# Kernel optimization log

Hardware: AMD Instinct MI355X
Metric: run time of the kernel (lower is better)

The kernel has to match this reference:

```python
import jax, jax.numpy as jnp
import numpy as np
from jax import lax

B, T, H, OUT = 2048, 512, 128, 64  # batch, lookback, hidden, horizon


def _p(k, shape):
    return jax.random.normal(k, shape, jnp.float32) * 0.1


def setup_inputs() -> dict:
    key = jax.random.key(0)
    ks = jax.random.split(key, 19)
    d = {"x": jax.random.normal(ks[0], (B, T), jnp.float32)}
    i = 1
    for pre in ("enc", "dec"):
        for l in range(2):
            insz = 1 if l == 0 else H
            d[f"{pre}_Wih{l}"] = _p(ks[i], (4 * H, insz)); i += 1
            d[f"{pre}_Whh{l}"] = _p(ks[i], (4 * H, H)); i += 1
            d[f"{pre}_bih{l}"] = _p(ks[i], (4 * H,)); i += 1
            d[f"{pre}_bhh{l}"] = _p(ks[i], (4 * H,)); i += 1
    d["lin_W"] = _p(ks[17], (1, H))
    d["lin_b"] = _p(ks[18], (1,))
    return d


def _cell(x, h, c, Wih, Whh, bih, bhh):
    # PyTorch LSTM gate order: i, f, g, o
    gates = x @ Wih.T + h @ Whh.T + bih + bhh  # [B, 4H]
    i, f, g, o = jnp.split(gates, 4, axis=-1)
    c = jax.nn.sigmoid(f) * c + jax.nn.sigmoid(i) * jnp.tanh(g)
    h = jax.nn.sigmoid(o) * jnp.tanh(c)
    return h, c


def _layer(xs, Wih, Whh, bih, bhh):
    # xs: [T, B, in] -> (ys [T, B, H], final (h, c))
    b = xs.shape[1]
    h0 = jnp.zeros((b, Whh.shape[1]), xs.dtype)
    def step(carry, x):
        h, c = _cell(x, carry[0], carry[1], Wih, Whh, bih, bhh)
        return (h, c), h
    (h, c), ys = lax.scan(step, (h0, h0), xs)
    return ys, (h, c)


def reference(x,
              enc_Wih0, enc_Whh0, enc_bih0, enc_bhh0,
              enc_Wih1, enc_Whh1, enc_bih1, enc_bhh1,
              dec_Wih0, dec_Whh0, dec_bih0, dec_bhh0,
              dec_Wih1, dec_Whh1, dec_bih1, dec_bhh1,
              lin_W, lin_b):
    xs = x.T[:, :, None]  # [T, B, 1]
    ys0, (h0, c0) = _layer(xs, enc_Wih0, enc_Whh0, enc_bih0, enc_bhh0)
    _,   (h1, c1) = _layer(ys0, enc_Wih1, enc_Whh1, enc_bih1, enc_bhh1)

    inp0 = x[:, -1:]  # [B, 1] last observed price
    def dec_step(carry, _):
        inp, a, b_, h, c = carry
        a, b_ = _cell(inp, a, b_, dec_Wih0, dec_Whh0, dec_bih0, dec_bhh0)
        h, c = _cell(a, h, c, dec_Wih1, dec_Whh1, dec_bih1, dec_bhh1)
        pred = h @ lin_W.T + lin_b  # [B, 1]
        return (pred, a, b_, h, c), pred[:, 0]

    _, preds = lax.scan(dec_step, (inp0, h0, c0, h1, c1), None, length=OUT)
    return preds.T  # [B, OUT]
```

## Files before the change

kernel.cpp:

```cpp
#include <hip/hip_runtime.h>


typedef _Float16 half_t;
typedef _Float16 f16x8 __attribute__((ext_vector_type(8)));
typedef float    f32x4 __attribute__((ext_vector_type(4)));

#define BT   8
#define H    128
#define T    512
#define OUTS 64

__device__ __forceinline__ float sigm(float x)   { return 1.0f / (1.0f + __expf(-x)); }
__device__ __forceinline__ float tanh_f(float x) { return 2.0f / (1.0f + __expf(-2.0f * x)) - 1.0f; }

__device__ __forceinline__ void mfma_a(f32x4& d, f16x8 a, const f16x8& b) {
  asm("v_mfma_f32_16x16x32_f16 %0, %1, %2, %0" : "+v"(d) : "v"(a), "a"(b));
}
__device__ __forceinline__ void mfma_v(f32x4& d, f16x8 a, const f16x8& b) {
  asm("v_mfma_f32_16x16x32_f16 %0, %1, %2, %0" : "+v"(d) : "v"(a), "v"(b));
}

__device__ __forceinline__ f16x8 lda(const half_t* buf, int col, int kg, int kb) {
  int b  = col >> 1;
  int bc = (kb * 64 + kg * 16) ^ (b << 4);
  return *(const f16x8*)((const char*)buf + b * 256 + bc);
}

__device__ __forceinline__ void wr_h(half_t* hb, int b, int j, float h) {
  int bc = (j * 2) ^ (b << 4);
  *(half_t*)((char*)hb + b * 256 + bc) = (half_t)h;
}

template <int M>
__device__ __forceinline__ void pass_a(f32x4 (&acc)[2][4], const f16x8 (&wa)[2][4][2][4],
                                       const half_t* buf, int col, int kg) {
#pragma unroll
  for (int kb = 0; kb < 4; kb++) {
    f16x8 a = lda(buf, col, kg, kb);
#pragma unroll
    for (int jt = 0; jt < 2; jt++)
#pragma unroll
      for (int q = 0; q < 4; q++)
        mfma_a(acc[jt][q], a, wa[M][q][jt][kb]);
  }
}

__device__ __forceinline__ void pass_v(f32x4 (&acc)[2][4], const f16x8 (&wv2)[4][2][4],
                                       const half_t* buf, int col, int kg) {
#pragma unroll
  for (int kb = 0; kb < 4; kb++) {
    f16x8 a = lda(buf, col, kg, kb);
#pragma unroll
    for (int jt = 0; jt < 2; jt++)
#pragma unroll
      for (int q = 0; q < 4; q++)
        mfma_v(acc[jt][q], a, wv2[q][jt][kb]);
  }
}

__device__ __forceinline__ void zacc(f32x4 (&acc)[2][4]) {
#pragma unroll
  for (int jt = 0; jt < 2; jt++)
#pragma unroll
    for (int q = 0; q < 4; q++) acc[jt][q] = (f32x4){0.f, 0.f, 0.f, 0.f};
}

__device__ __forceinline__ void load_wa(f16x8 (&wa)[2][4][2][4], const half_t* w16,
                                        int base, int wv, int col, int kg) {
#pragma unroll
  for (int m = 0; m < 2; m++)
#pragma unroll
    for (int q = 0; q < 4; q++)
#pragma unroll
      for (int jt = 0; jt < 2; jt++)
#pragma unroll
        for (int kb = 0; kb < 4; kb++) {
          wa[m][q][jt][kb] = *(const f16x8*)(w16 + (size_t)(base + m) * 65536 +
                                             (size_t)(q * 128 + wv * 32 + jt * 16 + col) * 128 +
                                             kb * 32 + kg * 8);
          asm("" : "+a"(wa[m][q][jt][kb]));
        }
}

__device__ __forceinline__ void load_wv(f16x8 (&wv2)[4][2][4], const half_t* w16,
                                        int base, int wv, int col, int kg) {
#pragma unroll
  for (int q = 0; q < 4; q++)
#pragma unroll
    for (int jt = 0; jt < 2; jt++)
#pragma unroll
      for (int kb = 0; kb < 4; kb++)
        wv2[q][jt][kb] = *(const f16x8*)(w16 + (size_t)(base + 2) * 65536 +
                                         (size_t)(q * 128 + wv * 32 + jt * 16 + col) * 128 +
                                         kb * 32 + kg * 8);
}

__global__ void prep_kernel(const float* m0, const float* m1, const float* m2,
                            const float* m3, const float* m4, const float* m5,
                            const float* ba0, const float* bb0, const float* ba1, const float* bb1,
                            const float* ba2, const float* bb2, const float* ba3, const float* bb3,
                            const float* encWih0, const float* decWih0,
                            half_t* w16, float* biasT, float* xwT) {
  int i = blockIdx.x * 256 + threadIdx.x;
  if (i < 6 * 65536) {
    int m = i >> 16, e = i & 65535;
    const float* src = (m == 0) ? m0 : (m == 1) ? m1 : (m == 2) ? m2
                     : (m == 3) ? m3 : (m == 4) ? m4 : m5;
    w16[i] = (half_t)src[e];
  }
  if (i < 2048) {
    int set = i >> 9, wi = i & 511, q = wi >> 7, jh = wi & 127;
    const float* A  = (set == 0) ? ba0 : (set == 1) ? ba1 : (set == 2) ? ba2 : ba3;
    const float* Bv = (set == 0) ? bb0 : (set == 1) ? bb1 : (set == 2) ? bb2 : bb3;
    biasT[set * 512 + jh * 4 + q] = A[wi] + Bv[wi];
  }
  if (i < 1024) {
    int ph = i >> 9, wi = i & 511, q = wi >> 7, jh = wi & 127;
    xwT[ph * 512 + jh * 4 + q] = (ph ? decWih0 : encWih0)[wi];
  }
}

__global__ __launch_bounds__(256, 1)
void lstm_all(const float* __restrict__ x,
              const float* __restrict__ linW,
              const float* __restrict__ linb,
              const half_t* __restrict__ w16,
              const float* __restrict__ biasTg,
              const float* __restrict__ xwTg,
              float* __restrict__ out)
{
  __shared__ alignas(16) half_t h0b[2][BT * H];
  __shared__ alignas(16) half_t h1b[2][BT * H];
  __shared__ float xch[BT * 64];
  __shared__ float h1f[BT * H];
  __shared__ float linWs[H];
  __shared__ float pp[256];
  __shared__ float predbuf[BT];

  const int tid  = threadIdx.x;
  const int wv   = tid >> 6;
  const int lane = tid & 63;
  const int col  = lane & 15;
  const int kg   = lane >> 4;
  const int b0   = blockIdx.x * BT;

  for (int z = tid; z < 1024; z += 256) {
    ((unsigned*)h0b)[z] = 0u; ((unsigned*)h1b)[z] = 0u;
  }
  if (tid < H) linWs[tid] = linW[tid];

  f16x8 wa[2][4][2][4];
  f16x8 wv2[4][2][4];
  load_wa(wa, w16, 0, wv, col, kg);
  load_wv(wv2, w16, 0, wv, col, kg);

  float b0r[2][4], b1r[2][4], xwr[2][4];
#pragma unroll
  for (int jt = 0; jt < 2; jt++) {
    const int jj = wv * 32 + jt * 16 + col;
#pragma unroll
    for (int q = 0; q < 4; q++) {
      b0r[jt][q] = biasTg[jj * 4 + q];
      b1r[jt][q] = biasTg[512 + jj * 4 + q];
      xwr[jt][q] = xwTg[jj * 4 + q];
    }
  }

  float c0[2][2] = {{0, 0}, {0, 0}};
  float c1[2][2] = {{0, 0}, {0, 0}};
  int p = 0;
  __syncthreads();

  for (int tc = 0; tc < 8; tc++) {
    for (int e = tid; e < BT * 64; e += 256)
      xch[e] = x[(size_t)(b0 + (e >> 6)) * T + tc * 64 + (e & 63)];
    __syncthreads();
    for (int ti = 0; ti < 64; ti++) {
      const int np = p ^ 1;
      f32x4 acc[2][4];
      zacc(acc);
      pass_a<0>(acc, wa, h0b[p], col, kg);
#pragma unroll
      for (int jt = 0; jt < 2; jt++) {
        const int jj = wv * 32 + jt * 16 + col;
#pragma unroll
        for (int s = 0; s < 2; s++) {
          const int b = 2 * kg + s;
          const int e = 2 * s;
          float xv = xch[b * 64 + ti];
          float gi = acc[jt][0][e] + b0r[jt][0] + xv * xwr[jt][0];
          float gf = acc[jt][1][e] + b0r[jt][1] + xv * xwr[jt][1];
          float gg = acc[jt][2][e] + b0r[jt][2] + xv * xwr[jt][2];
          float go = acc[jt][3][e] + b0r[jt][3] + xv * xwr[jt][3];
          float cn = sigm(gf) * c0[jt][s] + sigm(gi) * tanh_f(gg);
          c0[jt][s] = cn;
          wr_h(h0b[np], b, jj, sigm(go) * tanh_f(cn));
        }
      }
      __syncthreads();
      zacc(acc);
      pass_v(acc, wv2, h1b[p], col, kg);
      pass_a<1>(acc, wa, h0b[np], col, kg);
#pragma unroll
      for (int jt = 0; jt < 2; jt++) {
        const int jj = wv * 32 + jt * 16 + col;
#pragma unroll
        for (int s = 0; s < 2; s++) {
          const int b = 2 * kg + s;
          const int e = 2 * s;
          float gi = acc[jt][0][e] + b1r[jt][0];
          float gf = acc[jt][1][e] + b1r[jt][1];
          float gg = acc[jt][2][e] + b1r[jt][2];
          float go = acc[jt][3][e] + b1r[jt][3];
          float cn = sigm(gf) * c1[jt][s] + sigm(gi) * tanh_f(gg);
          c1[jt][s] = cn;
          wr_h(h1b[np], b, jj, sigm(go) * tanh_f(cn));
        }
      }
      __syncthreads();
      p = np;
    }
  }

  load_wa(wa, w16, 3, wv, col, kg);
  load_wv(wv2, w16, 3, wv, col, kg);
#pragma unroll
  for (int jt = 0; jt < 2; jt++) {
    const int jj = wv * 32 + jt * 16 + col;
#pragma unroll
    for (int q = 0; q < 4; q++) {
      b0r[jt][q] = biasTg[1024 + jj * 4 + q];
      b1r[jt][q] = biasTg[1536 + jj * 4 + q];
      xwr[jt][q] = xwTg[512 + jj * 4 + q];
    }
  }
  const float lb = linb[0];
  if (tid < BT) predbuf[tid] = x[(size_t)(b0 + tid) * T + (T - 1)];
  __syncthreads();

  for (int so = 0; so < OUTS; so++) {
    const int np = p ^ 1;
    f32x4 acc[2][4];
    zacc(acc);
    pass_a<0>(acc, wa, h0b[p], col, kg);
#pragma unroll
    for (int jt = 0; jt < 2; jt++) {
      const int jj = wv * 32 + jt * 16 + col;
#pragma unroll
      for (int s = 0; s < 2; s++) {
        const int b = 2 * kg + s;
        const int e = 2 * s;
        float xv = predbuf[b];
        float gi = acc[jt][0][e] + b0r[jt][0] + xv * xwr[jt][0];
        float gf = acc[jt][1][e] + b0r[jt][1] + xv * xwr[jt][1];
        float gg = acc[jt][2][e] + b0r[jt][2] + xv * xwr[jt][2];
        float go = acc[jt][3][e] + b0r[jt][3] + xv * xwr[jt][3];
        float cn = sigm(gf) * c0[jt][s] + sigm(gi) * tanh_f(gg);
        c0[jt][s] = cn;
        wr_h(h0b[np], b, jj, sigm(go) * tanh_f(cn));
      }
    }
    __syncthreads();
    zacc(acc);
    pass_v(acc, wv2, h1b[p], col, kg);
    pass_a<1>(acc, wa, h0b[np], col, kg);
#pragma unroll
    for (int jt = 0; jt < 2; jt++) {
      const int jj = wv * 32 + jt * 16 + col;
#pragma unroll
      for (int s = 0; s < 2; s++) {
        const int b = 2 * kg + s;
        const int e = 2 * s;
        float cn = sigm(acc[jt][1][e] + b1r[jt][1]) * c1[jt][s]
                 + sigm(acc[jt][0][e] + b1r[jt][0]) * tanh_f(acc[jt][2][e] + b1r[jt][2]);
        c1[jt][s] = cn;
        float hn = sigm(acc[jt][3][e] + b1r[jt][3]) * tanh_f(cn);
        wr_h(h1b[np], b, jj, hn);
        h1f[b * H + jj] = hn;
      }
    }
    __syncthreads();
    {
      int r = tid >> 5, seg = tid & 31;
      float pv = 0.0f;
#pragma unroll
      for (int kk = 0; kk < 4; kk++) pv += h1f[r * H + seg * 4 + kk] * linWs[seg * 4 + kk];
      pp[tid] = pv;
    }
    __syncthreads();
    if (tid < BT) {
      float pv = lb;
#pragma unroll
      for (int g2 = 0; g2 < 32; g2++) pv += pp[tid * 32 + g2];
      predbuf[tid] = pv;
      out[(size_t)(b0 + tid) * OUTS + so] = pv;
    }
    __syncthreads();
    p = np;
  }
}

extern "C" void kernel_launch(void* const* d_in, const int* in_sizes, int n_in,
                              void* d_out, int out_size, void* d_ws, size_t ws_size,
                              hipStream_t stream) {
  const float* x        = (const float*)d_in[0];
  const float* encWih0  = (const float*)d_in[1];
  const float* encWhh0  = (const float*)d_in[2];
  const float* encbih0  = (const float*)d_in[3];
  const float* encbhh0  = (const float*)d_in[4];
  const float* encWih1  = (const float*)d_in[5];
  const float* encWhh1  = (const float*)d_in[6];
  const float* encbih1  = (const float*)d_in[7];
  const float* encbhh1  = (const float*)d_in[8];
  const float* decWih0  = (const float*)d_in[9];
  const float* decWhh0  = (const float*)d_in[10];
  const float* decbih0  = (const float*)d_in[11];
  const float* decbhh0  = (const float*)d_in[12];
  const float* decWih1  = (const float*)d_in[13];
  const float* decWhh1  = (const float*)d_in[14];
  const float* decbih1  = (const float*)d_in[15];
  const float* decbhh1  = (const float*)d_in[16];
  const float* linW     = (const float*)d_in[17];
  const float* linb     = (const float*)d_in[18];

  half_t* w16  = (half_t*)d_ws;
  float*  biasT = (float*)((char*)d_ws + (size_t)6 * 65536 * 2);
  float*  xwT   = biasT + 2048;

  prep_kernel<<<1536, 256, 0, stream>>>(encWhh0, encWih1, encWhh1, decWhh0, decWih1, decWhh1,
                                        encbih0, encbhh0, encbih1, encbhh1,
                                        decbih0, decbhh0, decbih1, decbhh1,
                                        encWih0, decWih0, w16, biasT, xwT);
  lstm_all<<<256, 256, 0, stream>>>(x, linW, linb, w16, biasT, xwT, (float*)d_out);
}
```

Before: 1.496 ms.

## Skew encoder layers so layer1 step t runs with layer0 step t+1

Restructures the encoder recurrence as a wavefront: in each iteration, layer 1 computes step S from h0[S] while layer 0 computes step S+1 from the same buffer. The two passes then share one barrier per step instead of two, with a prologue for layer 0's first step and an epilogue for layer 1's last step. The x chunk is stored transposed so the eight batch values for a time step sit next to each other. Ping-pong buffer indices for the two layers now drift apart, so the decoder tracks separate parities p0 and p1.

```diff
diff --git a/kernel.cpp b/kernel.cpp
--- a/kernel.cpp
+++ b/kernel.cpp
@@ -131,7 +131,7 @@
 {
   __shared__ alignas(16) half_t h0b[2][BT * H];
   __shared__ alignas(16) half_t h1b[2][BT * H];
-  __shared__ float xch[BT * 64];
+  __shared__ float xch[64 * BT];
   __shared__ float h1f[BT * H];
   __shared__ float linWs[H];
   __shared__ float pp[256];
@@ -168,59 +168,117 @@
 
   float c0[2][2] = {{0, 0}, {0, 0}};
   float c1[2][2] = {{0, 0}, {0, 0}};
-  int p = 0;
+
+  for (int e = tid; e < BT * 64; e += 256) {
+    int b = e >> 6, j = e & 63;
+    xch[j * 8 + b] = x[(size_t)(b0 + b) * T + j];
+  }
   __syncthreads();
 
-  for (int tc = 0; tc < 8; tc++) {
-    for (int e = tid; e < BT * 64; e += 256)
-      xch[e] = x[(size_t)(b0 + (e >> 6)) * T + tc * 64 + (e & 63)];
-    __syncthreads();
-    for (int ti = 0; ti < 64; ti++) {
-      const int np = p ^ 1;
-      f32x4 acc[2][4];
-      zacc(acc);
-      pass_a<0>(acc, wa, h0b[p], col, kg);
-#pragma unroll
-      for (int jt = 0; jt < 2; jt++) {
-        const int jj = wv * 32 + jt * 16 + col;
-#pragma unroll
-        for (int s = 0; s < 2; s++) {
-          const int b = 2 * kg + s;
-          const int e = 2 * s;
-          float xv = xch[b * 64 + ti];
-          float gi = acc[jt][0][e] + b0r[jt][0] + xv * xwr[jt][0];
-          float gf = acc[jt][1][e] + b0r[jt][1] + xv * xwr[jt][1];
-          float gg = acc[jt][2][e] + b0r[jt][2] + xv * xwr[jt][2];
-          float go = acc[jt][3][e] + b0r[jt][3] + xv * xwr[jt][3];
-          float cn = sigm(gf) * c0[jt][s] + sigm(gi) * tanh_f(gg);
-          c0[jt][s] = cn;
-          wr_h(h0b[np], b, jj, sigm(go) * tanh_f(cn));
-        }
+  {
+    f32x4 acc[2][4];
+    zacc(acc);
+    pass_a<0>(acc, wa, h0b[0], col, kg);
+#pragma unroll
+    for (int jt = 0; jt < 2; jt++) {
+      const int jj = wv * 32 + jt * 16 + col;
+#pragma unroll
+      for (int s = 0; s < 2; s++) {
+        const int b = 2 * kg + s;
+        const int e = 2 * s;
+        float xv = xch[0 * 8 + b];
+        float gi = acc[jt][0][e] + b0r[jt][0] + xv * xwr[jt][0];
+        float gf = acc[jt][1][e] + b0r[jt][1] + xv * xwr[jt][1];
+        float gg = acc[jt][2][e] + b0r[jt][2] + xv * xwr[jt][2];
+        float go = acc[jt][3][e] + b0r[jt][3] + xv * xwr[jt][3];
+        float cn = sigm(gf) * c0[jt][s] + sigm(gi) * tanh_f(gg);
+        c0[jt][s] = cn;
+        wr_h(h0b[1], b, jj, sigm(go) * tanh_f(cn));
+      }
+    }
+  }
+  __syncthreads();
+  int p = 1;
+
+  for (int S = 0; S < 511; S++) {
+    if (((S + 1) & 63) == 0) {
+      const int ch = (S + 1) >> 6;
+      for (int e = tid; e < BT * 64; e += 256) {
+        int b = e >> 6, j = e & 63;
+        xch[j * 8 + b] = x[(size_t)(b0 + b) * T + ch * 64 + j];
       }
       __syncthreads();
-      zacc(acc);
-      pass_v(acc, wv2, h1b[p], col, kg);
-      pass_a<1>(acc, wa, h0b[np], col, kg);
-#pragma unroll
-      for (int jt = 0; jt < 2; jt++) {
-        const int jj = wv * 32 + jt * 16 + col;
-#pragma unroll
-        for (int s = 0; s < 2; s++) {
-          const int b = 2 * kg + s;
-          const int e = 2 * s;
-          float gi = acc[jt][0][e] + b1r[jt][0];
-          float gf = acc[jt][1][e] + b1r[jt][1];
-          float gg = acc[jt][2][e] + b1r[jt][2];
-          float go = acc[jt][3][e] + b1r[jt][3];
-          float cn = sigm(gf) * c1[jt][s] + sigm(gi) * tanh_f(gg);
-          c1[jt][s] = cn;
-          wr_h(h1b[np], b, jj, sigm(go) * tanh_f(cn));
-        }
-      }
-      __syncthreads();
-      p = np;
-    }
-  }
+    }
+    const int np = p ^ 1;
+    f32x4 acc[2][4];
+    zacc(acc);
+    pass_v(acc, wv2, h1b[p], col, kg);
+    pass_a<1>(acc, wa, h0b[p], col, kg);
+#pragma unroll
+    for (int jt = 0; jt < 2; jt++) {
+      const int jj = wv * 32 + jt * 16 + col;
+#pragma unroll
+      for (int s = 0; s < 2; s++) {
+        const int b = 2 * kg + s;
+        const int e = 2 * s;
+        float gi = acc[jt][0][e] + b1r[jt][0];
+        float gf = acc[jt][1][e] + b1r[jt][1];
+        float gg = acc[jt][2][e] + b1r[jt][2];
+        float go = acc[jt][3][e] + b1r[jt][3];
+        float cn = sigm(gf) * c1[jt][s] + sigm(gi) * tanh_f(gg);
+        c1[jt][s] = cn;
+        wr_h(h1b[np], b, jj, sigm(go) * tanh_f(cn));
+      }
+    }
+    zacc(acc);
+    pass_a<0>(acc, wa, h0b[p], col, kg);
+#pragma unroll
+    for (int jt = 0; jt < 2; jt++) {
+      const int jj = wv * 32 + jt * 16 + col;
+#pragma unroll
+      for (int s = 0; s < 2; s++) {
+        const int b = 2 * kg + s;
+        const int e = 2 * s;
+        float xv = xch[((S + 1) & 63) * 8 + b];
+        float gi = acc[jt][0][e] + b0r[jt][0] + xv * xwr[jt][0];
+        float gf = acc[jt][1][e] + b0r[jt][1] + xv * xwr[jt][1];
+        float gg = acc[jt][2][e] + b0r[jt][2] + xv * xwr[jt][2];
+        float go = acc[jt][3][e] + b0r[jt][3] + xv * xwr[jt][3];
+        float cn = sigm(gf) * c0[jt][s] + sigm(gi) * tanh_f(gg);
+        c0[jt][s] = cn;
+        wr_h(h0b[np], b, jj, sigm(go) * tanh_f(cn));
+      }
+    }
+    __syncthreads();
+    p = np;
+  }
+
+  {
+    const int np = p ^ 1;
+    f32x4 acc[2][4];
+    zacc(acc);
+    pass_v(acc, wv2, h1b[p], col, kg);
+    pass_a<1>(acc, wa, h0b[p], col, kg);
+#pragma unroll
+    for (int jt = 0; jt < 2; jt++) {
+      const int jj = wv * 32 + jt * 16 + col;
+#pragma unroll
+      for (int s = 0; s < 2; s++) {
+        const int b = 2 * kg + s;
+        const int e = 2 * s;
+        float gi = acc[jt][0][e] + b1r[jt][0];
+        float gf = acc[jt][1][e] + b1r[jt][1];
+        float gg = acc[jt][2][e] + b1r[jt][2];
+        float go = acc[jt][3][e] + b1r[jt][3];
+        float cn = sigm(gf) * c1[jt][s] + sigm(gi) * tanh_f(gg);
+        c1[jt][s] = cn;
+        wr_h(h1b[np], b, jj, sigm(go) * tanh_f(cn));
+      }
+    }
+    __syncthreads();
+  }
+  int p0 = p;
+  int p1 = p ^ 1;
 
   load_wa(wa, w16, 3, wv, col, kg);
   load_wv(wv2, w16, 3, wv, col, kg);
@@ -239,10 +297,10 @@
   __syncthreads();
 
   for (int so = 0; so < OUTS; so++) {
-    const int np = p ^ 1;
+    const int n0 = p0 ^ 1, n1 = p1 ^ 1;
     f32x4 acc[2][4];
     zacc(acc);
-    pass_a<0>(acc, wa, h0b[p], col, kg);
+    pass_a<0>(acc, wa, h0b[p0], col, kg);
 #pragma unroll
     for (int jt = 0; jt < 2; jt++) {
       const int jj = wv * 32 + jt * 16 + col;
@@ -257,13 +315,13 @@
         float go = acc[jt][3][e] + b0r[jt][3] + xv * xwr[jt][3];
         float cn = sigm(gf) * c0[jt][s] + sigm(gi) * tanh_f(gg);
         c0[jt][s] = cn;
-        wr_h(h0b[np], b, jj, sigm(go) * tanh_f(cn));
-      }
-    }
-    __syncthreads();
-    zacc(acc);
-    pass_v(acc, wv2, h1b[p], col, kg);
-    pass_a<1>(acc, wa, h0b[np], col, kg);
+        wr_h(h0b[n0], b, jj, sigm(go) * tanh_f(cn));
+      }
+    }
+    __syncthreads();
+    zacc(acc);
+    pass_v(acc, wv2, h1b[p1], col, kg);
+    pass_a<1>(acc, wa, h0b[n0], col, kg);
 #pragma unroll
     for (int jt = 0; jt < 2; jt++) {
       const int jj = wv * 32 + jt * 16 + col;
@@ -275,7 +333,7 @@
                  + sigm(acc[jt][0][e] + b1r[jt][0]) * tanh_f(acc[jt][2][e] + b1r[jt][2]);
         c1[jt][s] = cn;
         float hn = sigm(acc[jt][3][e] + b1r[jt][3]) * tanh_f(cn);
-        wr_h(h1b[np], b, jj, hn);
+        wr_h(h1b[n1], b, jj, hn);
         h1f[b * H + jj] = hn;
       }
     }
@@ -296,7 +354,7 @@
       out[(size_t)(b0 + tid) * OUTS + so] = pv;
     }
     __syncthreads();
-    p = np;
+    p0 = n0; p1 = n1;
   }
 }
 
```

New measurement: 1.313 ms, median of 2. 1.14x faster.
